# Kernel tuning notes

Measured on AMD Instinct MI355X. Metric: run time of the kernel, lower is better.

The kernel has to match this reference:

```python
import jax, jax.numpy as jnp
import numpy as np

N, D = 8192, 1024
NUM_CLASSES = 128
PPC = 4  # prototypes per class
P = NUM_CLASSES * PPC
ALPHA = 1.0
EPS = 1e-9


def setup_inputs() -> dict:
    key = jax.random.key(0)
    k1, k2, k3 = jax.random.split(key, 3)
    x = jax.random.normal(k1, (N, D), dtype=jnp.float32)
    y = jax.random.randint(k2, (N,), 0, NUM_CLASSES, dtype=jnp.int64)
    prototypes = jax.random.normal(k3, (P, D), dtype=jnp.float32)
    return {"x": x, "y": y, "t_value": 1, "prototypes": prototypes}


def reference(x, y, t_value, prototypes):
    # prototype labels: i // PPC
    proto_labels = jnp.arange(P, dtype=y.dtype) // PPC  # [P]

    x_sq = jnp.sum(x * x, axis=1, keepdims=True)          # [N,1]
    p_sq = jnp.sum(prototypes * prototypes, axis=1)       # [P]
    dist = x_sq + p_sq[None, :] - 2.0 * (x @ prototypes.T)  # [N,P]

    correct_mask = proto_labels[None, :] == y[:, None]    # [N,P]
    inf = jnp.array(jnp.inf, dtype=dist.dtype)
    d1 = jnp.min(jnp.where(correct_mask, dist, inf), axis=1)   # [N]
    d2 = jnp.min(jnp.where(correct_mask, inf, dist), axis=1)   # [N]

    mu = (d1 - d2) / (d1 + d2 + EPS)
    alpha = jnp.log(1.0 + jnp.asarray(t_value, dtype=dist.dtype)) / ALPHA
    return jnp.mean(jax.nn.sigmoid(alpha * mu))
```

## Files before the change

### kernel.cpp

```cpp
#include <hip/hip_runtime.h>
#include <hip/hip_bf16.h>
#include <math.h>
#include <stdint.h>

#define NS 8192
#define DD 1024
#define NP 512
#define BK 64
#define MT 64
#define NT 128
#define NSTEP (DD / BK)
#define NPARTS 8
#define EPSF 1e-9f
#define BIGF 3.0e38f

typedef __attribute__((ext_vector_type(8))) short bf16x8;
typedef __attribute__((ext_vector_type(4))) float f32x4;

__device__ inline unsigned short f32_to_bf16(float f) {
    uint32_t u = __builtin_bit_cast(uint32_t, f);
    uint32_t r = (u + 0x7FFFu + ((u >> 16) & 1u)) >> 16;
    return (unsigned short)r;
}

__global__ __launch_bounds__(256) void prep_kernel(
    const float* __restrict__ x, const float* __restrict__ protos,
    unsigned short* __restrict__ xb, unsigned short* __restrict__ pb,
    float* __restrict__ xsq, float* __restrict__ psq)
{
    int row = blockIdx.x;
    const float* src;
    unsigned short* dstb;
    float* dsts;
    if (row < NS) {
        src = x + (size_t)row * DD; dstb = xb + (size_t)row * DD; dsts = xsq + row;
    } else {
        int r = row - NS;
        src = protos + (size_t)r * DD; dstb = pb + (size_t)r * DD; dsts = psq + r;
    }
    int t = threadIdx.x;
    float4 v = ((const float4*)src)[t];
    float ss = v.x * v.x + v.y * v.y + v.z * v.z + v.w * v.w;
    ushort4 o;
    o.x = f32_to_bf16(v.x); o.y = f32_to_bf16(v.y);
    o.z = f32_to_bf16(v.z); o.w = f32_to_bf16(v.w);
    ((ushort4*)dstb)[t] = o;
    for (int off = 32; off; off >>= 1) ss += __shfl_down(ss, off);
    __shared__ float red[4];
    if ((t & 63) == 0) red[t >> 6] = ss;
    __syncthreads();
    if (t == 0) dsts[0] = red[0] + red[1] + red[2] + red[3];
}

__global__ __launch_bounds__(256, 2) void glvq_gemm(
    const unsigned short* __restrict__ xb, const unsigned short* __restrict__ pb,
    const float* __restrict__ xsq, const float* __restrict__ psq,
    const int* __restrict__ y,
    float* __restrict__ d1p, float* __restrict__ d2p)
{
    __shared__ unsigned short As[3][MT * BK];
    __shared__ unsigned short Bs[3][NT * BK];

    const int tid  = threadIdx.x;
    const int lane = tid & 63;
    const int wid  = tid >> 6;
    const int wr = wid >> 1;
    const int wc = wid & 1;
    const int d    = blockIdx.x;
    const int xcd  = d & 7;
    const int slot = d >> 3;
    const int mb   = xcd * 16 + (slot & 15);
    const int nb   = slot >> 4;
    const int m0   = mb * MT;
    const int n0   = nb * NT;

    const int srow   = lane >> 3;
    const int scol16 = (lane & 7) ^ srow;
    const int sub = lane & 15, g = lane >> 4;

    f32x4 acc[2][4] = {};

    auto stage = [&](int buf, int kt) {
        const int k0 = kt * BK;
#pragma unroll
        for (int j = 0; j < 2; ++j) {
            const int c = wid * 2 + j;
            const unsigned short* ga = xb + (size_t)(m0 + c * 8 + srow) * DD + k0 + scol16 * 8;
            __builtin_amdgcn_global_load_lds(
                (const __attribute__((address_space(1))) void*)ga,
                (__attribute__((address_space(3))) void*)((char*)&As[buf][0] + c * 1024),
                16, 0, 0);
        }
#pragma unroll
        for (int j = 0; j < 4; ++j) {
            const int c = wid * 4 + j;
            const unsigned short* gb = pb + (size_t)(n0 + c * 8 + srow) * DD + k0 + scol16 * 8;
            __builtin_amdgcn_global_load_lds(
                (const __attribute__((address_space(1))) void*)gb,
                (__attribute__((address_space(3))) void*)((char*)&Bs[buf][0] + c * 1024),
                16, 0, 0);
        }
    };

    auto compute = [&](int buf) {
#pragma unroll
        for (int kk = 0; kk < 2; ++kk) {
            bf16x8 a[2], b[4];
#pragma unroll
            for (int m = 0; m < 2; ++m) {
                const int rowa = wr * 32 + m * 16 + sub;
                const int c16 = (kk * 4 + g) ^ (rowa & 7);
                a[m] = *(const bf16x8*)((const char*)&As[buf][0] + rowa * 128 + c16 * 16);
            }
#pragma unroll
            for (int n = 0; n < 4; ++n) {
                const int rowb = wc * 64 + n * 16 + sub;
                const int c16 = (kk * 4 + g) ^ (rowb & 7);
                b[n] = *(const bf16x8*)((const char*)&Bs[buf][0] + rowb * 128 + c16 * 16);
            }
#pragma unroll
            for (int m = 0; m < 2; ++m)
#pragma unroll
                for (int n = 0; n < 4; ++n)
                    acc[m][n] = __builtin_amdgcn_mfma_f32_16x16x32_bf16(a[m], b[n], acc[m][n], 0, 0, 0);
        }
    };

    stage(0, 0);
    stage(1, 1);

    int cb = 0, sb = 2;
#pragma unroll 1
    for (int kt = 0; kt < NSTEP - 2; ++kt) {
        asm volatile("s_waitcnt vmcnt(6)" ::: "memory");
        __builtin_amdgcn_s_barrier();
        stage(sb, kt + 2);
        __builtin_amdgcn_s_setprio(1);
        compute(cb);
        __builtin_amdgcn_s_setprio(0);
        cb = (cb == 2) ? 0 : cb + 1;
        sb = (sb == 2) ? 0 : sb + 1;
    }
    asm volatile("s_waitcnt vmcnt(6)" ::: "memory");
    __builtin_amdgcn_s_barrier();
    __builtin_amdgcn_s_setprio(1);
    compute(cb);
    __builtin_amdgcn_s_setprio(0);
    cb = (cb == 2) ? 0 : cb + 1;
    asm volatile("s_waitcnt vmcnt(0)" ::: "memory");
    __builtin_amdgcn_s_barrier();
    compute(cb);

    float psqv[4];
    int   lab[4];
#pragma unroll
    for (int n = 0; n < 4; ++n) {
        const int col = n0 + wc * 64 + n * 16 + sub;
        psqv[n] = psq[col];
        lab[n]  = col >> 2;
    }
    const int part = nb * 2 + wc;
#pragma unroll
    for (int m = 0; m < 2; ++m) {
#pragma unroll
        for (int r = 0; r < 4; ++r) {
            const int rl = wr * 32 + m * 16 + g * 4 + r;
            const float xs = xsq[m0 + rl];
            const int yy = y[m0 + rl];
            float d1 = BIGF, d2 = BIGF;
#pragma unroll
            for (int n = 0; n < 4; ++n) {
                const float dist = xs + psqv[n] - 2.0f * acc[m][n][r];
                if (lab[n] == yy) d1 = fminf(d1, dist);
                else              d2 = fminf(d2, dist);
            }
            for (int off = 8; off; off >>= 1) {
                d1 = fminf(d1, __shfl_xor(d1, off));
                d2 = fminf(d2, __shfl_xor(d2, off));
            }
            if (sub == 0) {
                d1p[part * NS + m0 + rl] = d1;
                d2p[part * NS + m0 + rl] = d2;
            }
        }
    }
}

__global__ __launch_bounds__(256) void finalize_kernel(
    const float* __restrict__ d1p, const float* __restrict__ d2p,
    const int* __restrict__ tval, float* __restrict__ bsum)
{
    const int row = blockIdx.x * 256 + threadIdx.x;
    float d1 = BIGF, d2 = BIGF;
#pragma unroll
    for (int p = 0; p < NPARTS; ++p) {
        d1 = fminf(d1, d1p[p * NS + row]);
        d2 = fminf(d2, d2p[p * NS + row]);
    }
    const float mu = (d1 - d2) / (d1 + d2 + EPSF);
    const float alpha = logf(1.0f + (float)tval[0]);
    float s = 1.0f / (1.0f + expf(-alpha * mu));
    for (int off = 32; off; off >>= 1) s += __shfl_down(s, off);
    __shared__ float red[4];
    if ((threadIdx.x & 63) == 0) red[threadIdx.x >> 6] = s;
    __syncthreads();
    if (threadIdx.x == 0) bsum[blockIdx.x] = red[0] + red[1] + red[2] + red[3];
}

__global__ void final_sum(const float* __restrict__ bsum, float* __restrict__ out) {
    float s = (threadIdx.x < NS / 256) ? bsum[threadIdx.x] : 0.0f;
    for (int off = 32; off; off >>= 1) s += __shfl_down(s, off);
    if (threadIdx.x == 0) out[0] = s * (1.0f / (float)NS);
}

extern "C" void kernel_launch(void* const* d_in, const int* in_sizes, int n_in,
                              void* d_out, int out_size, void* d_ws, size_t ws_size,
                              hipStream_t stream) {
    const float* x      = (const float*)d_in[0];
    const int*   y      = (const int*)d_in[1];
    const int*   tval   = (const int*)d_in[2];
    const float* protos = (const float*)d_in[3];
    float* out = (float*)d_out;

    char* ws = (char*)d_ws;
    unsigned short* xb = (unsigned short*)(ws);
    unsigned short* pb = (unsigned short*)(ws + (size_t)NS * DD * 2);
    float* xsq  = (float*)(ws + (size_t)(NS + NP) * DD * 2);
    float* psq  = (float*)(ws + (size_t)(NS + NP) * DD * 2 + NS * 4);
    float* d1p  = (float*)(ws + (size_t)(NS + NP) * DD * 2 + (NS + NP) * 4);
    float* d2p  = d1p + (size_t)NPARTS * NS;
    float* bsum = d2p + (size_t)NPARTS * NS;

    prep_kernel<<<NS + NP, 256, 0, stream>>>(x, protos, xb, pb, xsq, psq);
    glvq_gemm<<<(NS / MT) * (NP / NT), 256, 0, stream>>>(xb, pb, xsq, psq, y, d1p, d2p);
    finalize_kernel<<<NS / 256, 256, 0, stream>>>(d1p, d2p, tval, bsum);
    final_sum<<<1, 64, 0, stream>>>(bsum, out);
}
```

Measured before the change: 37.42 us.

## Switch GEMM to double-buffered split A/B staging and fuse final reduction via atomics

The GEMM main loop moves from a three-buffer prefetch ring to a two-buffer scheme. It now reads fragments, issues the next B (then A) tile loads between the two k-halves, and separates the halves with barriers. Less LDS per block allows the launch bound to rise to three blocks per SU. The final_sum kernel is removed: finalize blocks atomically add scaled partial sums into an output zeroed by a memset. This trades a shorter prefetch distance and more barriers for occupancy, and swaps one kernel launch for a memset plus atomics, which makes the summation order nondeterministic.

```diff
diff --git a/kernel.cpp b/kernel.cpp
--- a/kernel.cpp
+++ b/kernel.cpp
@@ -52,14 +52,14 @@
     if (t == 0) dsts[0] = red[0] + red[1] + red[2] + red[3];
 }
 
-__global__ __launch_bounds__(256, 2) void glvq_gemm(
+__global__ __launch_bounds__(256, 3) void glvq_gemm(
     const unsigned short* __restrict__ xb, const unsigned short* __restrict__ pb,
     const float* __restrict__ xsq, const float* __restrict__ psq,
     const int* __restrict__ y,
     float* __restrict__ d1p, float* __restrict__ d2p)
 {
-    __shared__ unsigned short As[3][MT * BK];
-    __shared__ unsigned short Bs[3][NT * BK];
+    __shared__ unsigned short As[2][MT * BK];
+    __shared__ unsigned short Bs[2][NT * BK];
 
     const int tid  = threadIdx.x;
     const int lane = tid & 63;
@@ -80,7 +80,7 @@
 
     f32x4 acc[2][4] = {};
 
-    auto stage = [&](int buf, int kt) {
+    auto stageA = [&](int buf, int kt) {
         const int k0 = kt * BK;
 #pragma unroll
         for (int j = 0; j < 2; ++j) {
@@ -91,6 +91,9 @@
                 (__attribute__((address_space(3))) void*)((char*)&As[buf][0] + c * 1024),
                 16, 0, 0);
         }
+    };
+    auto stageB = [&](int buf, int kt) {
+        const int k0 = kt * BK;
 #pragma unroll
         for (int j = 0; j < 4; ++j) {
             const int c = wid * 4 + j;
@@ -102,54 +105,49 @@
         }
     };
 
-    auto compute = [&](int buf) {
-#pragma unroll
-        for (int kk = 0; kk < 2; ++kk) {
-            bf16x8 a[2], b[4];
-#pragma unroll
-            for (int m = 0; m < 2; ++m) {
-                const int rowa = wr * 32 + m * 16 + sub;
-                const int c16 = (kk * 4 + g) ^ (rowa & 7);
-                a[m] = *(const bf16x8*)((const char*)&As[buf][0] + rowa * 128 + c16 * 16);
-            }
-#pragma unroll
-            for (int n = 0; n < 4; ++n) {
-                const int rowb = wc * 64 + n * 16 + sub;
-                const int c16 = (kk * 4 + g) ^ (rowb & 7);
-                b[n] = *(const bf16x8*)((const char*)&Bs[buf][0] + rowb * 128 + c16 * 16);
-            }
-#pragma unroll
-            for (int m = 0; m < 2; ++m)
-#pragma unroll
-                for (int n = 0; n < 4; ++n)
-                    acc[m][n] = __builtin_amdgcn_mfma_f32_16x16x32_bf16(a[m], b[n], acc[m][n], 0, 0, 0);
-        }
-    };
-
-    stage(0, 0);
-    stage(1, 1);
-
-    int cb = 0, sb = 2;
+    auto readFrags = [&](int buf, int kk, bf16x8* a, bf16x8* b) {
+#pragma unroll
+        for (int m = 0; m < 2; ++m) {
+            const int rowa = wr * 32 + m * 16 + sub;
+            const int c16 = (kk * 4 + g) ^ (rowa & 7);
+            a[m] = *(const bf16x8*)((const char*)&As[buf][0] + rowa * 128 + c16 * 16);
+        }
+#pragma unroll
+        for (int n = 0; n < 4; ++n) {
+            const int rowb = wc * 64 + n * 16 + sub;
+            const int c16 = (kk * 4 + g) ^ (rowb & 7);
+            b[n] = *(const bf16x8*)((const char*)&Bs[buf][0] + rowb * 128 + c16 * 16);
+        }
+    };
+    auto mfma8 = [&](const bf16x8* a, const bf16x8* b) {
+        __builtin_amdgcn_s_setprio(1);
+#pragma unroll
+        for (int m = 0; m < 2; ++m)
+#pragma unroll
+            for (int n = 0; n < 4; ++n)
+                acc[m][n] = __builtin_amdgcn_mfma_f32_16x16x32_bf16(a[m], b[n], acc[m][n], 0, 0, 0);
+        __builtin_amdgcn_s_setprio(0);
+    };
+
+    stageB(0, 0);
+    stageA(0, 0);
+
 #pragma unroll 1
-    for (int kt = 0; kt < NSTEP - 2; ++kt) {
-        asm volatile("s_waitcnt vmcnt(6)" ::: "memory");
+    for (int kt = 0; kt < NSTEP; ++kt) {
+        const int buf = kt & 1;
+        asm volatile("s_waitcnt vmcnt(0)" ::: "memory");
         __builtin_amdgcn_s_barrier();
-        stage(sb, kt + 2);
-        __builtin_amdgcn_s_setprio(1);
-        compute(cb);
-        __builtin_amdgcn_s_setprio(0);
-        cb = (cb == 2) ? 0 : cb + 1;
-        sb = (sb == 2) ? 0 : sb + 1;
-    }
-    asm volatile("s_waitcnt vmcnt(6)" ::: "memory");
-    __builtin_amdgcn_s_barrier();
-    __builtin_amdgcn_s_setprio(1);
-    compute(cb);
-    __builtin_amdgcn_s_setprio(0);
-    cb = (cb == 2) ? 0 : cb + 1;
-    asm volatile("s_waitcnt vmcnt(0)" ::: "memory");
-    __builtin_amdgcn_s_barrier();
-    compute(cb);
+        bf16x8 a0[2], b0[4];
+        readFrags(buf, 0, a0, b0);
+        if (kt < NSTEP - 1) stageB(buf ^ 1, kt + 1);
+        __builtin_amdgcn_s_barrier();
+        mfma8(a0, b0);
+        bf16x8 a1[2], b1[4];
+        readFrags(buf, 1, a1, b1);
+        if (kt < NSTEP - 1) stageA(buf ^ 1, kt + 1);
+        __builtin_amdgcn_s_barrier();
+        mfma8(a1, b1);
+    }
 
     float psqv[4];
     int   lab[4];
@@ -188,7 +186,7 @@
 
 __global__ __launch_bounds__(256) void finalize_kernel(
     const float* __restrict__ d1p, const float* __restrict__ d2p,
-    const int* __restrict__ tval, float* __restrict__ bsum)
+    const int* __restrict__ tval, float* __restrict__ out)
 {
     const int row = blockIdx.x * 256 + threadIdx.x;
     float d1 = BIGF, d2 = BIGF;
@@ -204,13 +202,8 @@
     __shared__ float red[4];
     if ((threadIdx.x & 63) == 0) red[threadIdx.x >> 6] = s;
     __syncthreads();
-    if (threadIdx.x == 0) bsum[blockIdx.x] = red[0] + red[1] + red[2] + red[3];
-}
-
-__global__ void final_sum(const float* __restrict__ bsum, float* __restrict__ out) {
-    float s = (threadIdx.x < NS / 256) ? bsum[threadIdx.x] : 0.0f;
-    for (int off = 32; off; off >>= 1) s += __shfl_down(s, off);
-    if (threadIdx.x == 0) out[0] = s * (1.0f / (float)NS);
+    if (threadIdx.x == 0)
+        atomicAdd(out, (red[0] + red[1] + red[2] + red[3]) * (1.0f / (float)NS));
 }
 
 extern "C" void kernel_launch(void* const* d_in, const int* in_sizes, int n_in,
@@ -229,10 +222,9 @@
     float* psq  = (float*)(ws + (size_t)(NS + NP) * DD * 2 + NS * 4);
     float* d1p  = (float*)(ws + (size_t)(NS + NP) * DD * 2 + (NS + NP) * 4);
     float* d2p  = d1p + (size_t)NPARTS * NS;
-    float* bsum = d2p + (size_t)NPARTS * NS;
-
+
+    (void)hipMemsetAsync(d_out, 0, sizeof(float), stream);
     prep_kernel<<<NS + NP, 256, 0, stream>>>(x, protos, xb, pb, xsq, psq);
     glvq_gemm<<<(NS / MT) * (NP / NT), 256, 0, stream>>>(xb, pb, xsq, psq, y, d1p, d2p);
-    finalize_kernel<<<NS / 256, 256, 0, stream>>>(d1p, d2p, tval, bsum);
-    final_sum<<<1, 64, 0, stream>>>(bsum, out);
-}
+    finalize_kernel<<<NS / 256, 256, 0, stream>>>(d1p, d2p, tval, out);
+}
```

After: 41.79 us. 1.12x slower.
